# Optimization experiments

Measured on AMD Instinct MI355X. Metric: run time of the kernel, lower is better.

## Reference

```python
import jax, jax.numpy as jnp
import numpy as np

jax.config.update("jax_enable_x64", True)

DIM = 4
SUPEROP = 16
GAMMA = 1.0 / 88e-6  # 1 / TAU_EFF_53S


def _build_constants():
    g = np.array([1, 0], dtype=complex)
    r = np.array([0, 1], dtype=complex)
    s_gr = np.outer(g, r)
    s_rg = np.outer(r, g)
    n_r = np.outer(r, r)
    I2 = np.eye(2)
    s_gr1 = np.kron(s_gr, I2); s_rg1 = np.kron(s_rg, I2); n1 = np.kron(n_r, I2)
    s_gr2 = np.kron(I2, s_gr); s_rg2 = np.kron(I2, s_rg); n2 = np.kron(I2, n_r)
    H_drive = 0.5 * (s_rg1 + s_gr1 + s_rg2 + s_gr2)
    n_rr = n1 @ n2
    # decay superoperator: sum_k L_k (x) L_k* - 0.5 (L_k^dag L_k (x) I + I (x) (L_k^dag L_k)^T)
    I4 = np.eye(DIM)
    decay = np.zeros((SUPEROP, SUPEROP), dtype=complex)
    for c in (np.sqrt(GAMMA) * s_gr1, np.sqrt(GAMMA) * s_gr2):
        cdc = c.conj().T @ c
        decay += np.kron(c, c.conj()) - 0.5 * (np.kron(cdc, I4) + np.kron(I4, cdc.T))
    return (jnp.asarray(H_drive, jnp.complex128), jnp.asarray(n1, jnp.complex128),
            jnp.asarray(n2, jnp.complex128), jnp.asarray(n_rr, jnp.complex128),
            jnp.asarray(decay, jnp.complex128))


_H_DRIVE, _N1, _N2, _NRR, _DECAY = _build_constants()


def setup_inputs() -> dict:
    key = jax.random.key(0)
    ks = jax.random.split(key, 6)
    B = 65536
    names = ["Omega", "Delta", "delta_doppler_1", "delta_doppler_2", "delta_phase", "V_vdW"]
    return {n: jax.random.normal(k, (B,), dtype=jnp.float32) for n, k in zip(names, ks)}


def _liouvillian(Omega, Delta, dd1, dd2, dph, V):
    # build_hamiltonian: (batch,4,4) complex128
    Om = Omega.astype(jnp.float64)[:, None, None]
    D1 = (Delta + dd1 + dph).astype(jnp.float64)[:, None, None]
    D2 = (Delta + dd2 + dph).astype(jnp.float64)[:, None, None]
    Vv = V.astype(jnp.float64)[:, None, None]
    H = Om * _H_DRIVE - D1 * _N1 - D2 * _N2 + Vv * _NRR  # (b,4,4)
    I4 = jnp.eye(DIM, dtype=H.dtype)
    b = H.shape[0]
    # kron(H, I): (b,4,1,4,1)*(4,1,4) broadcast -> (b,4,4,4,4) -> (b,16,16)
    H_kron_I = (H[:, :, None, :, None] * I4[None, :, None, :]).reshape(b, SUPEROP, SUPEROP)
    HT = jnp.swapaxes(H, -1, -2)
    I_kron_HT = (I4[:, None, :, None] * HT[:, None, :, None, :]).reshape(b, SUPEROP, SUPEROP)
    return -1j * (H_kron_I - I_kron_HT) + _DECAY


def reference(Omega, Delta, delta_doppler_1, delta_doppler_2, delta_phase, V_vdW):
    return _liouvillian(Omega, Delta, delta_doppler_1, delta_doppler_2, delta_phase, V_vdW)
```

## Files before the change

kernel.cpp:

```cpp
#include <hip/hip_runtime.h>


#define GAMMA_F 11363.636363636364f

typedef float fx4 __attribute__((ext_vector_type(4)));

__device__ __forceinline__ float Hxy(int x, int y, float om2, float D1, float D2, float V) {
    if (x == y) {
        float d = 0.0f;
        if (x & 2) d -= D1;
        if (x & 1) d -= D2;
        if (x == 3) d += V;
        return d;
    }
    int t = x ^ y;
    return (t == 1 || t == 2) ? om2 : 0.0f;
}

__device__ __forceinline__ float decay_rc(int r, int c) {
    int i = r >> 2, j = r & 3, k = c >> 2, l = c & 3;
    float d = 0.0f;
    if (r == c)
        d = -0.5f * GAMMA_F * (float)((i >> 1) + (i & 1) + (j >> 1) + (j & 1));
    if (i < 2 && j < 2 && k == i + 2 && l == j + 2) d += GAMMA_F;
    if (!(i & 1) && !(j & 1) && k == i + 1 && l == j + 1) d += GAMMA_F;
    return d;
}

__device__ __forceinline__ fx4 elem_pair(int e, float om2, float D1, float D2, float V) {
    int r  = e >> 3;
    int c0 = (e & 7) << 1;
    int i = r >> 2, j = r & 3;
    fx4 o;
    {
        int c = c0, k = c >> 2, l = c & 3;
        float im = 0.0f;
        if (j == l) im -= Hxy(i, k, om2, D1, D2, V);
        if (i == k) im += Hxy(j, l, om2, D1, D2, V);
        o.x = decay_rc(r, c);
        o.y = im;
    }
    {
        int c = c0 + 1, k = c >> 2, l = c & 3;
        float im = 0.0f;
        if (j == l) im -= Hxy(i, k, om2, D1, D2, V);
        if (i == k) im += Hxy(j, l, om2, D1, D2, V);
        o.z = decay_rc(r, c);
        o.w = im;
    }
    return o;
}

__global__ __launch_bounds__(256) void lindblad_cplx(
        const float* __restrict__ Om, const float* __restrict__ De,
        const float* __restrict__ dd1, const float* __restrict__ dd2,
        const float* __restrict__ dph, const float* __restrict__ Vv,
        fx4* __restrict__ out, int nthreads, int n4) {
    int g = blockIdx.x * blockDim.x + threadIdx.x;
    if (g >= nthreads) return;

    int b = __builtin_amdgcn_readfirstlane(g >> 6);

    float om2 = 0.5f * Om[b];
    float bd  = De[b] + dph[b];
    float D1  = bd + dd1[b];
    float D2  = bd + dd2[b];
    float V   = Vv[b];

    int e0   = g & 63;
    int idx0 = (b << 7) + e0;
    int idx1 = idx0 + 64;

    fx4 o0 = elem_pair(e0,      om2, D1, D2, V);
    fx4 o1 = elem_pair(e0 + 64, om2, D1, D2, V);

    if (idx0 < n4) __builtin_nontemporal_store(o0, &out[idx0]);
    if (idx1 < n4) __builtin_nontemporal_store(o1, &out[idx1]);
}

__global__ __launch_bounds__(256) void lindblad_real(
        fx4* __restrict__ out, int n4) {
    int g = blockIdx.x * blockDim.x + threadIdx.x;
    if (g >= n4) return;
    int e = g & 63;
    int r = e >> 2;
    int c0 = (e & 3) << 2;
    fx4 o;
    o.x = decay_rc(r, c0 + 0);
    o.y = decay_rc(r, c0 + 1);
    o.z = decay_rc(r, c0 + 2);
    o.w = decay_rc(r, c0 + 3);
    __builtin_nontemporal_store(o, &out[g]);
}

extern "C" void kernel_launch(void* const* d_in, const int* in_sizes, int n_in,
                              void* d_out, int out_size, void* d_ws, size_t ws_size,
                              hipStream_t stream) {
    const float* Om  = (const float*)d_in[0];
    const float* De  = (const float*)d_in[1];
    const float* dd1 = (const float*)d_in[2];
    const float* dd2 = (const float*)d_in[3];
    const float* dph = (const float*)d_in[4];
    const float* dVv = (const float*)d_in[5];
    int B = in_sizes[0];

    const int block = 256;

    if (out_size == B * 256) {
        int n4 = out_size >> 2;
        int grid = (n4 + block - 1) / block;
        lindblad_real<<<grid, block, 0, stream>>>((fx4*)d_out, n4);
    } else {
        int n4 = out_size >> 2;
        int want4 = B * 128;
        if (n4 > want4) n4 = want4;
        int nthreads = B * 64;
        int grid = (nthreads + block - 1) / block;
        lindblad_cplx<<<grid, block, 0, stream>>>(Om, De, dd1, dd2, dph, dVv,
                                                  (fx4*)d_out, nthreads, n4);
    }
}
```

Before: 85.92 us.

## Use persistent grid-stride waves with hoisted per-lane coefficient tables

```diff
diff --git a/kernel.cpp b/kernel.cpp
--- a/kernel.cpp
+++ b/kernel.cpp
@@ -4,18 +4,6 @@
 #define GAMMA_F 11363.636363636364f
 
 typedef float fx4 __attribute__((ext_vector_type(4)));
-
-__device__ __forceinline__ float Hxy(int x, int y, float om2, float D1, float D2, float V) {
-    if (x == y) {
-        float d = 0.0f;
-        if (x & 2) d -= D1;
-        if (x & 1) d -= D2;
-        if (x == 3) d += V;
-        return d;
-    }
-    int t = x ^ y;
-    return (t == 1 || t == 2) ? om2 : 0.0f;
-}
 
 __device__ __forceinline__ float decay_rc(int r, int c) {
     int i = r >> 2, j = r & 3, k = c >> 2, l = c & 3;
@@ -27,55 +15,78 @@
     return d;
 }
 
-__device__ __forceinline__ fx4 elem_pair(int e, float om2, float D1, float D2, float V) {
-    int r  = e >> 3;
-    int c0 = (e & 7) << 1;
-    int i = r >> 2, j = r & 3;
-    fx4 o;
-    {
-        int c = c0, k = c >> 2, l = c & 3;
-        float im = 0.0f;
-        if (j == l) im -= Hxy(i, k, om2, D1, D2, V);
-        if (i == k) im += Hxy(j, l, om2, D1, D2, V);
-        o.x = decay_rc(r, c);
-        o.y = im;
-    }
-    {
-        int c = c0 + 1, k = c >> 2, l = c & 3;
-        float im = 0.0f;
-        if (j == l) im -= Hxy(i, k, om2, D1, D2, V);
-        if (i == k) im += Hxy(j, l, om2, D1, D2, V);
-        o.z = decay_rc(r, c);
-        o.w = im;
-    }
-    return o;
+__device__ __forceinline__ void im_coefs(int r, int c,
+        float& fAh, float& fAom, float& fBh, float& fBom) {
+    int i = r >> 2, j = r & 3, k = c >> 2, l = c & 3;
+    bool jl = (j == l), ik = (i == k);
+    int xik = i ^ k, xjl = j ^ l;
+    bool oik = (xik == 1) || (xik == 2);
+    bool ojl = (xjl == 1) || (xjl == 2);
+    fAh  = (jl && ik)          ? -1.0f : 0.0f;
+    fAom = (jl && !ik && oik)  ? -1.0f : 0.0f;
+    fBh  = (ik && jl)          ?  1.0f : 0.0f;
+    fBom = (ik && !jl && ojl)  ?  1.0f : 0.0f;
+}
+
+__device__ __forceinline__ void h_coefs(int x, float& cd1, float& cd2, float& cv) {
+    cd1 = (x & 2) ? -1.0f : 0.0f;
+    cd2 = (x & 1) ? -1.0f : 0.0f;
+    cv  = (x == 3) ? 1.0f : 0.0f;
 }
 
 __global__ __launch_bounds__(256) void lindblad_cplx(
         const float* __restrict__ Om, const float* __restrict__ De,
         const float* __restrict__ dd1, const float* __restrict__ dd2,
         const float* __restrict__ dph, const float* __restrict__ Vv,
-        fx4* __restrict__ out, int nthreads, int n4) {
-    int g = blockIdx.x * blockDim.x + threadIdx.x;
-    if (g >= nthreads) return;
+        fx4* __restrict__ out, int B, int n4, int nwaves) {
+    const int lane = threadIdx.x & 63;
+    const int wid  = __builtin_amdgcn_readfirstlane(
+        blockIdx.x * (blockDim.x >> 6) + (threadIdx.x >> 6));
 
-    int b = __builtin_amdgcn_readfirstlane(g >> 6);
+    const int r0 = lane >> 3;
+    const int c0 = (lane & 7) << 1;
+    const int r1 = r0 + 8;
+    const int i0 = r0 >> 2, j0 = r0 & 3;
+    const int i1 = r1 >> 2, j1 = r1 & 3;
 
-    float om2 = 0.5f * Om[b];
-    float bd  = De[b] + dph[b];
-    float D1  = bd + dd1[b];
-    float D2  = bd + dd2[b];
-    float V   = Vv[b];
+    const float re00 = decay_rc(r0, c0), re01 = decay_rc(r0, c0 + 1);
+    const float re10 = decay_rc(r1, c0), re11 = decay_rc(r1, c0 + 1);
 
-    int e0   = g & 63;
-    int idx0 = (b << 7) + e0;
-    int idx1 = idx0 + 64;
+    float a00h, a00o, b00h, b00o;  im_coefs(r0, c0,     a00h, a00o, b00h, b00o);
+    float a01h, a01o, b01h, b01o;  im_coefs(r0, c0 + 1, a01h, a01o, b01h, b01o);
+    float a10h, a10o, b10h, b10o;  im_coefs(r1, c0,     a10h, a10o, b10h, b10o);
+    float a11h, a11o, b11h, b11o;  im_coefs(r1, c0 + 1, a11h, a11o, b11h, b11o);
 
-    fx4 o0 = elem_pair(e0,      om2, D1, D2, V);
-    fx4 o1 = elem_pair(e0 + 64, om2, D1, D2, V);
+    float ci0_1, ci0_2, ci0_v;  h_coefs(i0, ci0_1, ci0_2, ci0_v);
+    float cj0_1, cj0_2, cj0_v;  h_coefs(j0, cj0_1, cj0_2, cj0_v);
+    float ci1_1, ci1_2, ci1_v;  h_coefs(i1, ci1_1, ci1_2, ci1_v);
+    float cj1_1, cj1_2, cj1_v;  h_coefs(j1, cj1_1, cj1_2, cj1_v);
 
-    if (idx0 < n4) __builtin_nontemporal_store(o0, &out[idx0]);
-    if (idx1 < n4) __builtin_nontemporal_store(o1, &out[idx1]);
+    for (int b = wid; b < B; b += nwaves) {
+        float om2 = 0.5f * Om[b];
+        float bd  = De[b] + dph[b];
+        float D1  = bd + dd1[b];
+        float D2  = bd + dd2[b];
+        float V   = Vv[b];
+
+        float hi0 = fmaf(ci0_v, V, fmaf(ci0_2, D2, ci0_1 * D1));
+        float hj0 = fmaf(cj0_v, V, fmaf(cj0_2, D2, cj0_1 * D1));
+        float hi1 = fmaf(ci1_v, V, fmaf(ci1_2, D2, ci1_1 * D1));
+        float hj1 = fmaf(cj1_v, V, fmaf(cj1_2, D2, cj1_1 * D1));
+
+        float im00 = fmaf(a00h, hi0, a00o * om2) + fmaf(b00h, hj0, b00o * om2);
+        float im01 = fmaf(a01h, hi0, a01o * om2) + fmaf(b01h, hj0, b01o * om2);
+        float im10 = fmaf(a10h, hi1, a10o * om2) + fmaf(b10h, hj1, b10o * om2);
+        float im11 = fmaf(a11h, hi1, a11o * om2) + fmaf(b11h, hj1, b11o * om2);
+
+        fx4 o0 = {re00, im00, re01, im01};
+        fx4 o1 = {re10, im10, re11, im11};
+
+        int idx0 = (b << 7) + lane;
+        int idx1 = idx0 + 64;
+        if (idx0 < n4) __builtin_nontemporal_store(o0, &out[idx0]);
+        if (idx1 < n4) __builtin_nontemporal_store(o1, &out[idx1]);
+    }
 }
 
 __global__ __launch_bounds__(256) void lindblad_real(
@@ -114,9 +125,10 @@
         int n4 = out_size >> 2;
         int want4 = B * 128;
         if (n4 > want4) n4 = want4;
-        int nthreads = B * 64;
-        int grid = (nthreads + block - 1) / block;
-        lindblad_cplx<<<grid, block, 0, stream>>>(Om, De, dd1, dd2, dph, dVv,
-                                                  (fx4*)d_out, nthreads, n4);
+        int nblocks = (B + 3) / 4;
+        if (nblocks > 2048) nblocks = 2048;
+        int nwaves = nblocks * (block / 64);
+        lindblad_cplx<<<nblocks, block, 0, stream>>>(Om, De, dd1, dd2, dph, dVv,
+                                                     (fx4*)d_out, B, n4, nwaves);
     }
 }
```

Result: no change. 85.12 us (-0.9%).
